# Kernel optimization log

Hardware: AMD Instinct MI355X
Metric: run time of the kernel (lower is better)

Reference implementation:

```python
import jax, jax.numpy as jnp
import numpy as np
from math import pi

N = 256        # in_features == out_features
BATCH = 131072


def givens_orthogonal(angles, n):
    """Build an n x n orthogonal matrix as the ordered product of Givens
    rotations G(i, j, theta_k) over pairs i < j in lexicographic order.
    Each rotation mixes rows i and j; applied sequentially via lax.scan."""
    ii, jj = np.triu_indices(n, 1)  # static pair order, len = n*(n-1)//2
    ii = jnp.asarray(ii, dtype=jnp.int32)
    jj = jnp.asarray(jj, dtype=jnp.int32)

    def body(M, t):
        i, j, th = t
        c, s = jnp.cos(th), jnp.sin(th)
        ri, rj = M[i], M[j]
        M = M.at[i].set(c * ri - s * rj)
        M = M.at[j].set(s * ri + c * rj)
        return M, None

    M0 = jnp.eye(n, dtype=angles.dtype)
    M, _ = jax.lax.scan(body, M0, (ii, jj, angles))
    return M


def setup_inputs() -> dict:
    key = jax.random.key(0)
    k1, k2, k3 = jax.random.split(key, 3)
    n_ang = N * (N - 1) // 2  # 32640
    return {
        "x": jax.random.normal(k1, (BATCH, N), dtype=jnp.float32),
        "Uweight": jax.random.uniform(k2, (n_ang,), minval=-pi / 2, maxval=pi / 2, dtype=jnp.float32),
        "Vweight": jax.random.uniform(k3, (n_ang,), minval=-pi / 2, maxval=pi / 2, dtype=jnp.float32),
        "Sweight": jnp.ones((N,), dtype=jnp.float32),
        "bias": jnp.zeros((N,), dtype=jnp.float32),
    }


def reference(x, Uweight, Vweight, Sweight, bias):
    # W = V @ diag(S) @ U^T  (SVD-parametrized weight, out x in)
    # y = x @ W^T + b = ((x @ U) * S) @ V^T + b   (square case in == out)
    U = givens_orthogonal(Uweight, N)  # (in, in) orthogonal
    V = givens_orthogonal(Vweight, N)  # (out, out) orthogonal
    return ((x @ U) * Sweight) @ V.T + bias
```

## Files before the change

kernel.cpp:

```cpp
#include <hip/hip_runtime.h>
#include <hip/hip_bf16.h>
#include <math.h>

#define NN 256
#define NSEG 32
#define MAT (NN*NN)

#define MATS0 0
#define MATS1 (MATS0 + 64*MAT)
#define WBT_OFF (MATS1 + 32*MAT)

static __device__ const int BD[NSEG+1] =
    {0,4,8,12,16,20,24,28,32,37,42,47,52,57,62,67,73,79,85,91,97,
     104,111,118,126,134,143,153,164,177,192,213,255};
#define CSL_CAP 1120

typedef __attribute__((ext_vector_type(8))) short short8;
typedef __attribute__((ext_vector_type(4))) float f32x4;

__device__ __forceinline__ short f2bf(float f) {
    __hip_bfloat16 h = __float2bfloat16(f);
    return *reinterpret_cast<short*>(&h);
}

#define BAR() do {                                              \
    asm volatile("s_waitcnt lgkmcnt(0)" ::: "memory");          \
    __builtin_amdgcn_s_barrier();                               \
    asm volatile("" ::: "memory");                              \
} while (0)

__global__ __launch_bounds__(64) void k_build(const float* __restrict__ au,
                                              const float* __restrict__ av,
                                              float* __restrict__ mats) {
    int b = blockIdx.x;
    int matid = b >> 7;
    int seg   = (b >> 2) & 31;
    int chunk = b & 3;
    int t = threadIdx.x;
    int c0 = chunk * 64;
    int i0 = BD[seg], i1 = BD[seg+1];
    float* outp = mats + (matid * NSEG + seg) * MAT;

    if (c0 + 64 <= i0) {
        for (int id = t; id < 4096; id += 64) {
            int row = id >> 4, c4 = (id & 15) * 4;
            float4 v = {0.f,0.f,0.f,0.f};
            int d = row - (c0 + c4);
            if (d >= 0 && d < 4) ((float*)&v)[d] = 1.0f;
            *(float4*)(outp + row*NN + c0 + c4) = v;
        }
        return;
    }

    __shared__ float M[NN * 64];
    __shared__ float2 csl[CSL_CAP];

    int kbase = 255*i0 - (i0*(i0-1))/2;
    int kend  = 255*i1 - (i1*(i1-1))/2;
    int nrot  = kend - kbase;
    const float* ang = (matid ? av : au) + kbase;
    for (int idx = t; idx < nrot; idx += 64) {
        float s, c;
        sincosf(ang[idx], &s, &c);
        float2 v = {c, s};
        csl[idx] = v;
    }
    int MR = NN - i0;
    for (int rr = 0; rr < MR; ++rr)
        M[rr*64 + t] = (i0 + rr == c0 + t) ? 1.0f : 0.0f;
    __syncthreads();

    int i = i0;
    while (i < i1) {
        int bs = i1 - i; if (bs > 4) bs = 4;
        float r[4];
#pragma unroll
        for (int k = 0; k < 4; ++k)
            if (k < bs) r[k] = M[(i + k - i0)*64 + t];

#pragma unroll
        for (int a = 0; a < 3; ++a)
#pragma unroll
            for (int b2 = a + 1; b2 < 4; ++b2)
                if (b2 < bs && i + b2 >= c0) {
                    int aa = i + a;
                    int idx = 255*aa - (aa*(aa-1))/2 + (b2 - a - 1) - kbase;
                    float2 cs = csl[idx];
                    float wv = cs.y*r[a] + cs.x*r[b2];
                    r[a]  = cs.x*r[a] - cs.y*r[b2];
                    r[b2] = wv;
                }

        int jblk = i + bs; if (jblk < c0) jblk = c0;
        int base[4];
#pragma unroll
        for (int k = 0; k < 4; ++k) {
            int a = i + k;
            base[k] = 255*a - (a*(a-1))/2 - a - 1 - kbase;
        }

        int j = jblk;
        int ngr = (NN - jblk) >> 2;
        float rjc[4]; float2 csc[4][4];
        if (ngr > 0) {
#pragma unroll
            for (int u = 0; u < 4; ++u) rjc[u] = M[(j + u - i0)*64 + t];
#pragma unroll
            for (int k = 0; k < 4; ++k)
                if (k < bs)
#pragma unroll
                    for (int u = 0; u < 4; ++u)
                        csc[k][u] = csl[base[k] + j + u];
        }
        for (int g = 0; g < ngr; ++g) {
            float rjn[4]; float2 csn[4][4];
            if (g + 1 < ngr) {
#pragma unroll
                for (int u = 0; u < 4; ++u) rjn[u] = M[(j + 4 + u - i0)*64 + t];
#pragma unroll
                for (int k = 0; k < 4; ++k)
                    if (k < bs)
#pragma unroll
                        for (int u = 0; u < 4; ++u)
                            csn[k][u] = csl[base[k] + j + 4 + u];
            }
#pragma unroll
            for (int u = 0; u < 4; ++u) {
                float rj = rjc[u];
#pragma unroll
                for (int k = 0; k < 4; ++k)
                    if (k < bs) {
                        float2 cs = csc[k][u];
                        float wv = cs.y*r[k] + cs.x*rj;
                        r[k] = cs.x*r[k] - cs.y*rj;
                        rj = wv;
                    }
                M[(j + u - i0)*64 + t] = rj;
            }
#pragma unroll
            for (int u = 0; u < 4; ++u) rjc[u] = rjn[u];
#pragma unroll
            for (int k = 0; k < 4; ++k)
#pragma unroll
                for (int u = 0; u < 4; ++u) csc[k][u] = csn[k][u];
            j += 4;
        }
        for (; j < NN; ++j) {
            float rj = M[(j - i0)*64 + t];
#pragma unroll
            for (int k = 0; k < 4; ++k)
                if (k < bs) {
                    float2 cs = csl[base[k] + j];
                    float wv = cs.y*r[k] + cs.x*rj;
                    r[k] = cs.x*r[k] - cs.y*rj;
                    rj = wv;
                }
            M[(j - i0)*64 + t] = rj;
        }
#pragma unroll
        for (int k = 0; k < 4; ++k)
            if (k < bs) M[(i + k - i0)*64 + t] = r[k];
        i += bs;
    }
    __syncthreads();

    for (int id = t; id < 4096; id += 64) {
        int row = id >> 4, c4 = (id & 15) * 4;
        float4 v;
        if (row < i0) {
            v = make_float4(0.f,0.f,0.f,0.f);
            int d = row - (c0 + c4);
            if (d >= 0 && d < 4) ((float*)&v)[d] = 1.0f;
        } else {
            v = *(const float4*)&M[(row - i0)*64 + c4];
        }
        *(float4*)(outp + row*NN + c0 + c4) = v;
    }
}

__device__ __forceinline__ void fold_body(const float* __restrict__ in,
                                          float* __restrict__ out,
                                          int nOut, int lg, int span,
                                          int b, int t) {
    int np2 = 2 * nOut;
    int m    = b & (np2 - 1);
    int tile = b >> lg;
    int side = (m >= nOut) ? 1 : 0;
    int q = m - side * nOut;
    const float* A = in + (side*np2 + 2*q + 1) * MAT;
    const float* B = in + (side*np2 + 2*q) * MAT;
    float* C = out + m * MAT;
    int i0A = BD[q * span + (span >> 1)];
    int r0 = (tile >> 2) * 64, c0 = (tile & 3) * 64;

    if (r0 + 64 <= i0A) {
#pragma unroll
        for (int u = 0; u < 4; ++u) {
            int id = u*256 + t;
            int rr = id >> 4, cc = (id & 15) * 4;
            *(float4*)(C + (r0+rr)*NN + c0 + cc) =
                *(const float4*)(B + (r0+rr)*NN + c0 + cc);
        }
        return;
    }

    int kstart = ((r0 < i0A) ? r0 : i0A) & ~31;
    int nt = (NN - kstart) >> 5;

    __shared__ float Ast[2][32][68];
    __shared__ float Bs [2][32][68];
    int tx = t & 15, ty = t >> 4;
    int arow = t >> 3, ak4 = t & 7;
    int bkr = t >> 4, bc4 = t & 15;

    float acc[4][4] = {};
    f32x4 pa0, pa1, pb0, pb1;
    {
        int kt = kstart;
        pa0 = *(const f32x4*)(A + (r0 + arow     )*NN + kt + ak4*4);
        pa1 = *(const f32x4*)(A + (r0 + arow + 32)*NN + kt + ak4*4);
        pb0 = *(const f32x4*)(B + (kt + bkr      )*NN + c0 + bc4*4);
        pb1 = *(const f32x4*)(B + (kt + bkr + 16 )*NN + c0 + bc4*4);
    }
    for (int it = 0; it < nt; ++it) {
        int cur = it & 1;
#pragma unroll
        for (int jj = 0; jj < 4; ++jj) {
            Ast[cur][ak4*4 + jj][arow]      = pa0[jj];
            Ast[cur][ak4*4 + jj][arow + 32] = pa1[jj];
        }
        *(f32x4*)&Bs[cur][bkr     ][bc4*4] = pb0;
        *(f32x4*)&Bs[cur][bkr + 16][bc4*4] = pb1;
        if (it + 1 < nt) {
            int k2 = kstart + (it+1)*32;
            pa0 = *(const f32x4*)(A + (r0 + arow     )*NN + k2 + ak4*4);
            pa1 = *(const f32x4*)(A + (r0 + arow + 32)*NN + k2 + ak4*4);
            pb0 = *(const f32x4*)(B + (k2 + bkr      )*NN + c0 + bc4*4);
            pb1 = *(const f32x4*)(B + (k2 + bkr + 16 )*NN + c0 + bc4*4);
        }
        BAR();
#pragma unroll 8
        for (int kk = 0; kk < 32; ++kk) {
            f32x4 a4 = *(const f32x4*)&Ast[cur][kk][ty*4];
            f32x4 b4 = *(const f32x4*)&Bs [cur][kk][tx*4];
#pragma unroll
            for (int rr = 0; rr < 4; ++rr)
#pragma unroll
                for (int cc = 0; cc < 4; ++cc)
                    acc[rr][cc] = fmaf(a4[rr], b4[cc], acc[rr][cc]);
        }
    }
#pragma unroll
    for (int rr = 0; rr < 4; ++rr) {
        float4 o = {acc[rr][0], acc[rr][1], acc[rr][2], acc[rr][3]};
        *(float4*)(C + (r0 + ty*4 + rr)*NN + c0 + tx*4) = o;
    }
}

__global__ __launch_bounds__(256) void k_fold1(const float* in, float* out)
{ fold_body(in, out, 16, 5,  2, blockIdx.x, threadIdx.x); }
__global__ __launch_bounds__(256) void k_fold2(const float* in, float* out)
{ fold_body(in, out,  8, 4,  4, blockIdx.x, threadIdx.x); }
__global__ __launch_bounds__(256) void k_fold3(const float* in, float* out)
{ fold_body(in, out,  4, 3,  8, blockIdx.x, threadIdx.x); }
__global__ __launch_bounds__(256) void k_fold4(const float* in, float* out)
{ fold_body(in, out,  2, 2, 16, blockIdx.x, threadIdx.x); }
__global__ __launch_bounds__(256) void k_fold5(const float* in, float* out)
{ fold_body(in, out,  1, 1, 32, blockIdx.x, threadIdx.x); }

__global__ __launch_bounds__(256) void k_wmatT(const float* __restrict__ U,
                                               const float* __restrict__ V,
                                               const float* __restrict__ S,
                                               unsigned short* __restrict__ Wbt) {
    int b = blockIdx.x;
    int n0 = (b >> 4) * 16, i0 = (b & 15) * 16;
    int t = threadIdx.x, ti = t & 15, tn = t >> 4;
    __shared__ float Us[16][260];
    __shared__ float Vs[16][260];
    {
        int rr = t >> 4, cc = (t & 15) * 16;
#pragma unroll
        for (int q = 0; q < 4; ++q) {
            float4 u = *(const float4*)(U + (i0+rr)*NN + cc + q*4);
            float4 s = *(const float4*)(S + cc + q*4);
            u.x *= s.x; u.y *= s.y; u.z *= s.z; u.w *= s.w;
            *(float4*)&Us[rr][cc+q*4] = u;
            *(float4*)&Vs[rr][cc+q*4] = *(const float4*)(V + (n0+rr)*NN + cc + q*4);
        }
    }
    __syncthreads();
    float acc = 0.f;
#pragma unroll 8
    for (int k4 = 0; k4 < 64; ++k4) {
        float4 uu = *(const float4*)&Us[ti][k4*4];
        float4 vv = *(const float4*)&Vs[tn][k4*4];
        acc += uu.x*vv.x + uu.y*vv.y + uu.z*vv.z + uu.w*vv.w;
    }
    Wbt[(n0+tn)*NN + (i0+ti)] = (unsigned short)f2bf(acc);
}

__global__ __launch_bounds__(512, 4) void k_mm(const float* __restrict__ x,
                                               const unsigned short* __restrict__ Wbt,
                                               const float* __restrict__ bias,
                                               float* __restrict__ out) {
    int t = threadIdx.x;
    int w = t >> 6, l = t & 63, l15 = l & 15, lg = l >> 4;
    int n0 = w * 32;

    __shared__ unsigned short Xs[2][8 * 512];

    long rowbase = (long)blockIdx.x * 256;
    int r = t & 15, m = t >> 4;
    int ksb = m >> 2;
    int lidx = r + 16 * (m & 3);

    const float* s0 = x + (rowbase + r) * NN + 8*m;
    float4 f0 = *(const float4*)(s0);
    float4 f1 = *(const float4*)(s0 + 4);

    short8 bfrag[2][8];
#pragma unroll
    for (int nt = 0; nt < 2; ++nt) {
        const unsigned short* wrow = Wbt + (n0 + nt*16 + l15) * NN + lg * 8;
#pragma unroll
        for (int ks = 0; ks < 8; ++ks)
            bfrag[nt][ks] = *(const short8*)(wrow + ks * 32);
    }
    float b0 = bias[n0 + l15];
    float b1 = bias[n0 + 16 + l15];

    for (int it = 0; it < 16; ++it) {
        int cur = it & 1;
        short8 h;
        h[0]=f2bf(f0.x); h[1]=f2bf(f0.y); h[2]=f2bf(f0.z); h[3]=f2bf(f0.w);
        h[4]=f2bf(f1.x); h[5]=f2bf(f1.y); h[6]=f2bf(f1.z); h[7]=f2bf(f1.w);
        *(short8*)&Xs[cur][ksb*512 + lidx*8] = h;
        if (it < 15) {
            const float* sn = x + (rowbase + (it+1)*16 + r) * NN + 8*m;
            f0 = *(const float4*)(sn);
            f1 = *(const float4*)(sn + 4);
        }
        BAR();

        f32x4 acc0 = {0.f,0.f,0.f,0.f}, acc1 = {0.f,0.f,0.f,0.f};
#pragma unroll
        for (int ks = 0; ks < 8; ++ks) {
            short8 af = *(const short8*)&Xs[cur][ks*512 + l*8];
            acc0 = __builtin_amdgcn_mfma_f32_16x16x32_bf16(af, bfrag[0][ks], acc0, 0, 0, 0);
            acc1 = __builtin_amdgcn_mfma_f32_16x16x32_bf16(af, bfrag[1][ks], acc1, 0, 0, 0);
        }
        float* op = out + (rowbase + it*16 + lg*4) * NN + n0 + l15;
#pragma unroll
        for (int rr = 0; rr < 4; ++rr) {
            __builtin_nontemporal_store(acc0[rr] + b0, op + rr * NN);
            __builtin_nontemporal_store(acc1[rr] + b1, op + rr * NN + 16);
        }
    }
}

extern "C" void kernel_launch(void* const* d_in, const int* in_sizes, int n_in,
                              void* d_out, int out_size, void* d_ws, size_t ws_size,
                              hipStream_t stream) {
    const float* x    = (const float*)d_in[0];
    const float* Uw   = (const float*)d_in[1];
    const float* Vw   = (const float*)d_in[2];
    const float* Sw   = (const float*)d_in[3];
    const float* bias = (const float*)d_in[4];
    float* out = (float*)d_out;
    float* ws  = (float*)d_ws;

    k_build<<<256, 64, 0, stream>>>(Uw, Vw, ws + MATS0);
    k_fold1<<<16*32, 256, 0, stream>>>(ws + MATS0, ws + MATS1);
    k_fold2<<<16*16, 256, 0, stream>>>(ws + MATS1, ws + MATS0);
    k_fold3<<<16* 8, 256, 0, stream>>>(ws + MATS0, ws + MATS1);
    k_fold4<<<16* 4, 256, 0, stream>>>(ws + MATS1, ws + MATS0);
    k_fold5<<<16* 2, 256, 0, stream>>>(ws + MATS0, ws + MATS1);
    k_wmatT<<<256, 256, 0, stream>>>(ws + MATS1, ws + MATS1 + MAT, Sw,
                                     (unsigned short*)(ws + WBT_OFF));
    k_mm<<<512, 512, 0, stream>>>(x, (unsigned short*)(ws + WBT_OFF), bias, out);
}
```

Before: 189.2 us.

## Fuse fold stages and W build into one persistent kernel with grid barriers

Replaces five fold kernels plus the W-transpose kernel with a single 512-block kernel that separates the stages with atomic-counter grid barriers, and zeroes the counters with a memset before each launch. The goal is to remove the launch gaps and tail drain between the small dependent stages. In exchange, every block must be co-resident for the spin barrier to be safe, and idle blocks spin through the later stages that use only a few tiles. Shared memory is now a single manual buffer reused by the fold and transpose units.

```diff
diff --git a/kernel.cpp b/kernel.cpp
--- a/kernel.cpp
+++ b/kernel.cpp
@@ -9,11 +9,14 @@
 #define MATS0 0
 #define MATS1 (MATS0 + 64*MAT)
 #define WBT_OFF (MATS1 + 32*MAT)
+#define BAR_OFF (WBT_OFF + 16384)
 
 static __device__ const int BD[NSEG+1] =
     {0,4,8,12,16,20,24,28,32,37,42,47,52,57,62,67,73,79,85,91,97,
      104,111,118,126,134,143,153,164,177,192,213,255};
 #define CSL_CAP 1120
+
+#define FOLD_GRID 512
 
 typedef __attribute__((ext_vector_type(8))) short short8;
 typedef __attribute__((ext_vector_type(4))) float f32x4;
@@ -28,6 +31,20 @@
     __builtin_amdgcn_s_barrier();                               \
     asm volatile("" ::: "memory");                              \
 } while (0)
+
+__device__ __forceinline__ void gridbar(unsigned* cnt, int id) {
+    __syncthreads();
+    if (threadIdx.x == 0) {
+        __threadfence();
+        __hip_atomic_fetch_add(&cnt[id], 1u, __ATOMIC_RELAXED,
+                               __HIP_MEMORY_SCOPE_AGENT);
+        while (__hip_atomic_load(&cnt[id], __ATOMIC_RELAXED,
+                                 __HIP_MEMORY_SCOPE_AGENT) < FOLD_GRID)
+            __builtin_amdgcn_s_sleep(8);
+        __threadfence();
+    }
+    __syncthreads();
+}
 
 __global__ __launch_bounds__(64) void k_build(const float* __restrict__ au,
                                               const float* __restrict__ av,
@@ -178,10 +195,10 @@
     }
 }
 
-__device__ __forceinline__ void fold_body(const float* __restrict__ in,
+__device__ __forceinline__ void fold_unit(const float* __restrict__ in,
                                           float* __restrict__ out,
                                           int nOut, int lg, int span,
-                                          int b, int t) {
+                                          int b, int t, unsigned char* smem) {
     int np2 = 2 * nOut;
     int m    = b & (np2 - 1);
     int tile = b >> lg;
@@ -207,8 +224,8 @@
     int kstart = ((r0 < i0A) ? r0 : i0A) & ~31;
     int nt = (NN - kstart) >> 5;
 
-    __shared__ float Ast[2][32][68];
-    __shared__ float Bs [2][32][68];
+    float (*Ast)[32][68] = (float(*)[32][68])smem;
+    float (*Bs )[32][68] = (float(*)[32][68])(smem + 17408);
     int tx = t & 15, ty = t >> 4;
     int arow = t >> 3, ak4 = t & 7;
     int bkr = t >> 4, bc4 = t & 15;
@@ -257,26 +274,15 @@
     }
 }
 
-__global__ __launch_bounds__(256) void k_fold1(const float* in, float* out)
-{ fold_body(in, out, 16, 5,  2, blockIdx.x, threadIdx.x); }
-__global__ __launch_bounds__(256) void k_fold2(const float* in, float* out)
-{ fold_body(in, out,  8, 4,  4, blockIdx.x, threadIdx.x); }
-__global__ __launch_bounds__(256) void k_fold3(const float* in, float* out)
-{ fold_body(in, out,  4, 3,  8, blockIdx.x, threadIdx.x); }
-__global__ __launch_bounds__(256) void k_fold4(const float* in, float* out)
-{ fold_body(in, out,  2, 2, 16, blockIdx.x, threadIdx.x); }
-__global__ __launch_bounds__(256) void k_fold5(const float* in, float* out)
-{ fold_body(in, out,  1, 1, 32, blockIdx.x, threadIdx.x); }
-
-__global__ __launch_bounds__(256) void k_wmatT(const float* __restrict__ U,
-                                               const float* __restrict__ V,
-                                               const float* __restrict__ S,
-                                               unsigned short* __restrict__ Wbt) {
-    int b = blockIdx.x;
+__device__ __forceinline__ void wmatT_unit(const float* __restrict__ U,
+                                           const float* __restrict__ V,
+                                           const float* __restrict__ S,
+                                           unsigned short* __restrict__ Wbt,
+                                           int b, int t, unsigned char* smem) {
     int n0 = (b >> 4) * 16, i0 = (b & 15) * 16;
-    int t = threadIdx.x, ti = t & 15, tn = t >> 4;
-    __shared__ float Us[16][260];
-    __shared__ float Vs[16][260];
+    int ti = t & 15, tn = t >> 4;
+    float (*Us)[260] = (float(*)[260])smem;
+    float (*Vs)[260] = (float(*)[260])(smem + 16640);
     {
         int rr = t >> 4, cc = (t & 15) * 16;
 #pragma unroll
@@ -297,6 +303,27 @@
         acc += uu.x*vv.x + uu.y*vv.y + uu.z*vv.z + uu.w*vv.w;
     }
     Wbt[(n0+tn)*NN + (i0+ti)] = (unsigned short)f2bf(acc);
+}
+
+__global__ __launch_bounds__(256, 4)
+void k_foldall(const float* __restrict__ S, float* __restrict__ ws,
+               unsigned short* __restrict__ Wbt, unsigned* __restrict__ cnt) {
+    __shared__ __align__(16) unsigned char smem[34816];
+    int b = blockIdx.x, t = threadIdx.x;
+    float* m0 = ws + MATS0;
+    float* m1 = ws + MATS1;
+
+    fold_unit(m0, m1, 16, 5,  2, b, t, smem);
+    gridbar(cnt, 0);
+    if (b < 256) fold_unit(m1, m0,  8, 4,  4, b, t, smem);
+    gridbar(cnt, 1);
+    if (b < 128) fold_unit(m0, m1,  4, 3,  8, b, t, smem);
+    gridbar(cnt, 2);
+    if (b <  64) fold_unit(m1, m0,  2, 2, 16, b, t, smem);
+    gridbar(cnt, 3);
+    if (b <  32) fold_unit(m0, m1,  1, 1, 32, b, t, smem);
+    gridbar(cnt, 4);
+    if (b < 256) wmatT_unit(m1, m1 + MAT, S, Wbt, b, t, smem);
 }
 
 __global__ __launch_bounds__(512, 4) void k_mm(const float* __restrict__ x,
@@ -369,13 +396,10 @@
     float* out = (float*)d_out;
     float* ws  = (float*)d_ws;
 
+    hipMemsetAsync(ws + BAR_OFF, 0, 64, stream);
     k_build<<<256, 64, 0, stream>>>(Uw, Vw, ws + MATS0);
-    k_fold1<<<16*32, 256, 0, stream>>>(ws + MATS0, ws + MATS1);
-    k_fold2<<<16*16, 256, 0, stream>>>(ws + MATS1, ws + MATS0);
-    k_fold3<<<16* 8, 256, 0, stream>>>(ws + MATS0, ws + MATS1);
-    k_fold4<<<16* 4, 256, 0, stream>>>(ws + MATS1, ws + MATS0);
-    k_fold5<<<16* 2, 256, 0, stream>>>(ws + MATS0, ws + MATS1);
-    k_wmatT<<<256, 256, 0, stream>>>(ws + MATS1, ws + MATS1 + MAT, Sw,
-                                     (unsigned short*)(ws + WBT_OFF));
+    k_foldall<<<FOLD_GRID, 256, 0, stream>>>(Sw, ws,
+                                             (unsigned short*)(ws + WBT_OFF),
+                                             (unsigned*)(ws + BAR_OFF));
     k_mm<<<512, 512, 0, stream>>>(x, (unsigned short*)(ws + WBT_OFF), bias, out);
 }
```

Result: slower. 374.7 us (+98.0%).

## Overlap x-to-bf16 conversion with Givens build and read bf16 x in GEMM

Applied to the files above, without the earlier changes.

Extra waves (threads 64-191) in the Givens-build kernel now convert x to bf16 into workspace, overlapping that conversion with the latency-bound rotation chain. The final GEMM then reads the half-size bf16 x instead of fp32. The block-wide barriers in the build are replaced with wave-local LDS waits, since the rotation work uses a single wave. This adds an extra full read and write of x, and it only takes effect if the workspace is large enough.

```diff
diff --git a/kernel.cpp b/kernel.cpp
--- a/kernel.cpp
+++ b/kernel.cpp
@@ -9,6 +9,8 @@
 #define MATS0 0
 #define MATS1 (MATS0 + 64*MAT)
 #define WBT_OFF (MATS1 + 32*MAT)
+#define XBF_OFF (WBT_OFF + 32768)
+#define WS_NEED_FLOATS (XBF_OFF + 16777216)
 
 static __device__ const int BD[NSEG+1] =
     {0,4,8,12,16,20,24,28,32,37,42,47,52,57,62,67,73,79,85,91,97,
@@ -29,14 +31,44 @@
     asm volatile("" ::: "memory");                              \
 } while (0)
 
-__global__ __launch_bounds__(64) void k_build(const float* __restrict__ au,
-                                              const float* __restrict__ av,
-                                              float* __restrict__ mats) {
+#define WAVE_LDS_FENCE() asm volatile("s_waitcnt lgkmcnt(0)" ::: "memory")
+
+__global__ __launch_bounds__(192) void k_build(const float* __restrict__ au,
+                                               const float* __restrict__ av,
+                                               float* __restrict__ mats,
+                                               const float* __restrict__ x,
+                                               unsigned short* __restrict__ xbf) {
     int b = blockIdx.x;
+    int t = threadIdx.x;
+
+    if (t >= 64) {
+        if (xbf != nullptr) {
+            int q = b * 128 + (t - 64);
+            for (int k = 0; k < 128; k += 4) {
+                long e[4]; float4 a[4], c[4];
+#pragma unroll
+                for (int j = 0; j < 4; ++j) {
+                    e[j] = ((long)q + (long)(k + j) * 32768) * 8;
+                    a[j] = *(const float4*)(x + e[j]);
+                    c[j] = *(const float4*)(x + e[j] + 4);
+                }
+#pragma unroll
+                for (int j = 0; j < 4; ++j) {
+                    short8 h;
+                    h[0]=f2bf(a[j].x); h[1]=f2bf(a[j].y);
+                    h[2]=f2bf(a[j].z); h[3]=f2bf(a[j].w);
+                    h[4]=f2bf(c[j].x); h[5]=f2bf(c[j].y);
+                    h[6]=f2bf(c[j].z); h[7]=f2bf(c[j].w);
+                    *(short8*)(xbf + e[j]) = h;
+                }
+            }
+        }
+        return;
+    }
+
     int matid = b >> 7;
     int seg   = (b >> 2) & 31;
     int chunk = b & 3;
-    int t = threadIdx.x;
     int c0 = chunk * 64;
     int i0 = BD[seg], i1 = BD[seg+1];
     float* outp = mats + (matid * NSEG + seg) * MAT;
@@ -68,7 +100,7 @@
     int MR = NN - i0;
     for (int rr = 0; rr < MR; ++rr)
         M[rr*64 + t] = (i0 + rr == c0 + t) ? 1.0f : 0.0f;
-    __syncthreads();
+    WAVE_LDS_FENCE();
 
     int i = i0;
     while (i < i1) {
@@ -162,7 +194,7 @@
             if (k < bs) M[(i + k - i0)*64 + t] = r[k];
         i += bs;
     }
-    __syncthreads();
+    WAVE_LDS_FENCE();
 
     for (int id = t; id < 4096; id += 64) {
         int row = id >> 4, c4 = (id & 15) * 4;
@@ -299,6 +331,60 @@
     Wbt[(n0+tn)*NN + (i0+ti)] = (unsigned short)f2bf(acc);
 }
 
+__global__ __launch_bounds__(512, 4) void k_mm_bf(const unsigned short* __restrict__ xbf,
+                                                  const unsigned short* __restrict__ Wbt,
+                                                  const float* __restrict__ bias,
+                                                  float* __restrict__ out) {
+    int t = threadIdx.x;
+    int w = t >> 6, l = t & 63, l15 = l & 15, lg = l >> 4;
+    int n0 = w * 32;
+
+    __shared__ unsigned short Xs[2][8 * 512];
+
+    long rowbase = (long)blockIdx.x * 256;
+    int r = t & 15, m = t >> 4;
+    int ksb = m >> 2;
+    int lidx = r + 16 * (m & 3);
+
+    const unsigned short* s0 = xbf + (rowbase + r) * NN + 8*m;
+    short8 f = *(const short8*)(s0);
+
+    short8 bfrag[2][8];
+#pragma unroll
+    for (int nt = 0; nt < 2; ++nt) {
+        const unsigned short* wrow = Wbt + (n0 + nt*16 + l15) * NN + lg * 8;
+#pragma unroll
+        for (int ks = 0; ks < 8; ++ks)
+            bfrag[nt][ks] = *(const short8*)(wrow + ks * 32);
+    }
+    float b0 = bias[n0 + l15];
+    float b1 = bias[n0 + 16 + l15];
+
+    for (int it = 0; it < 16; ++it) {
+        int cur = it & 1;
+        *(short8*)&Xs[cur][ksb*512 + lidx*8] = f;
+        if (it < 15) {
+            const unsigned short* sn = xbf + (rowbase + (it+1)*16 + r) * NN + 8*m;
+            f = *(const short8*)(sn);
+        }
+        BAR();
+
+        f32x4 acc0 = {0.f,0.f,0.f,0.f}, acc1 = {0.f,0.f,0.f,0.f};
+#pragma unroll
+        for (int ks = 0; ks < 8; ++ks) {
+            short8 af = *(const short8*)&Xs[cur][ks*512 + l*8];
+            acc0 = __builtin_amdgcn_mfma_f32_16x16x32_bf16(af, bfrag[0][ks], acc0, 0, 0, 0);
+            acc1 = __builtin_amdgcn_mfma_f32_16x16x32_bf16(af, bfrag[1][ks], acc1, 0, 0, 0);
+        }
+        float* op = out + (rowbase + it*16 + lg*4) * NN + n0 + l15;
+#pragma unroll
+        for (int rr = 0; rr < 4; ++rr) {
+            __builtin_nontemporal_store(acc0[rr] + b0, op + rr * NN);
+            __builtin_nontemporal_store(acc1[rr] + b1, op + rr * NN + 16);
+        }
+    }
+}
+
 __global__ __launch_bounds__(512, 4) void k_mm(const float* __restrict__ x,
                                                const unsigned short* __restrict__ Wbt,
                                                const float* __restrict__ bias,
@@ -369,7 +455,11 @@
     float* out = (float*)d_out;
     float* ws  = (float*)d_ws;
 
-    k_build<<<256, 64, 0, stream>>>(Uw, Vw, ws + MATS0);
+    bool fused = ws_size >= (size_t)WS_NEED_FLOATS * sizeof(float);
+    unsigned short* xbf = (unsigned short*)(ws + XBF_OFF);
+
+    k_build<<<256, 192, 0, stream>>>(Uw, Vw, ws + MATS0, x,
+                                     fused ? xbf : nullptr);
     k_fold1<<<16*32, 256, 0, stream>>>(ws + MATS0, ws + MATS1);
     k_fold2<<<16*16, 256, 0, stream>>>(ws + MATS1, ws + MATS0);
     k_fold3<<<16* 8, 256, 0, stream>>>(ws + MATS0, ws + MATS1);
@@ -377,5 +467,10 @@
     k_fold5<<<16* 2, 256, 0, stream>>>(ws + MATS0, ws + MATS1);
     k_wmatT<<<256, 256, 0, stream>>>(ws + MATS1, ws + MATS1 + MAT, Sw,
                                      (unsigned short*)(ws + WBT_OFF));
-    k_mm<<<512, 512, 0, stream>>>(x, (unsigned short*)(ws + WBT_OFF), bias, out);
-}
+    if (fused)
+        k_mm_bf<<<512, 512, 0, stream>>>(xbf, (unsigned short*)(ws + WBT_OFF),
+                                         bias, out);
+    else
+        k_mm<<<512, 512, 0, stream>>>(x, (unsigned short*)(ws + WBT_OFF),
+                                      bias, out);
+}
```

Result: slower. 200.6 us (+6.0%).
